# Optimization experiments

Hardware: AMD Instinct MI355X
Metric: run time of the kernel (lower is better)

## Reference

```python
import jax, jax.numpy as jnp
import numpy as np

N_NODES = 50000
N_EDGES = 800000
N_GRAPHS = 500
NFEAT = 128
NHID = 64
NLAYER = 3
BN_EPS = 1e-5


def setup_inputs() -> dict:
    key = jax.random.key(0)
    ks = jax.random.split(key, 8)
    x = jax.random.normal(ks[0], (N_NODES, NFEAT), dtype=jnp.float32)
    edge_index = jax.random.randint(ks[1], (2, N_EDGES), 0, N_NODES)
    batch = jnp.sort(jax.random.randint(ks[2], (N_NODES,), 0, N_GRAPHS))
    Wt = jax.random.normal(ks[3], (NFEAT, NHID), dtype=jnp.float32) / np.float32(np.sqrt(NFEAT))
    bt = jnp.zeros((NHID,), jnp.float32)
    gamma0 = jnp.ones((NHID,), jnp.float32)
    beta0 = jnp.zeros((NHID,), jnp.float32)
    W1 = jax.random.normal(ks[4], (NLAYER, NHID, NHID), dtype=jnp.float32) / np.float32(np.sqrt(NHID))
    W2 = jax.random.normal(ks[5], (NLAYER, NHID, NHID), dtype=jnp.float32) / np.float32(np.sqrt(NHID))
    gammas = jnp.ones((NLAYER, NHID), jnp.float32)
    betas = jnp.zeros((NLAYER, NHID), jnp.float32)
    return dict(x=x, edge_index=edge_index, batch=batch, Wt=Wt, bt=bt,
                gamma0=gamma0, beta0=beta0, W1=W1, W2=W2, gammas=gammas, betas=betas)


def _bn(h, g, b):
    # BatchNorm1d training-mode math: batch mean, biased variance
    mean = jnp.mean(h, axis=0)
    var = jnp.mean((h - mean) ** 2, axis=0)
    return (h - mean) * jax.lax.rsqrt(var + BN_EPS) * g + b


def _pool_mean(h, batch):
    s = jax.ops.segment_sum(h, batch, num_segments=N_GRAPHS)
    cnt = jax.ops.segment_sum(jnp.ones((h.shape[0], 1), h.dtype), batch, num_segments=N_GRAPHS)
    return s / jnp.maximum(cnt, 1.0)


def _embed_std(h, batch):
    m = _pool_mean(h, batch)                      # [G, nhid]
    s = jnp.sqrt(_pool_mean((h - m[batch]) ** 2, batch))
    return m, s


def reference(x, edge_index, batch, Wt, bt, gamma0, beta0, W1, W2, gammas, betas):
    src, dst = edge_index[0], edge_index[1]
    h = _bn(x @ Wt + bt, gamma0, beta0)           # transform: Linear + BN
    e0, s0 = _embed_std(h, batch)

    def step(h, p):
        w1, w2, g, b = p
        agg = jax.ops.segment_sum(h[src], dst, num_segments=N_NODES)  # GIN sum-aggregation
        z = (h + agg)                              # (1+eps)*x + agg, eps=0
        z = jax.nn.relu(z @ w1) @ w2               # GINConv nn: Linear-ReLU-Linear (no bias)
        z = _bn(jax.nn.relu(z), g, b)              # act then BN
        e, s = _embed_std(z, batch)
        return z, (e, s)

    _, (es, ss) = jax.lax.scan(step, h, (W1, W2, gammas, betas))
    graph_embeds = jnp.concatenate([e0[None], es], axis=0)  # [nlayer+1, G, nhid]
    graph_stds = jnp.concatenate([s0[None], ss], axis=0)
    return graph_embeds, graph_stds
```

## Files before the change

### kernel.cpp

```cpp
#include <hip/hip_runtime.h>
#include <hip/hip_bf16.h>

#define NN 50000
#define NE 800000
#define NG 500
#define NF 128
#define NH 64
#define NB 256
#define NPB 196
#define CAPB 4096
#define EPB 4096
#define NBLK ((NE + EPB - 1)/EPB)
#define CSR_LDS 2048
#define GBIN 8

typedef unsigned int u32;
typedef unsigned short u16;
typedef _Float16 h2 __attribute__((ext_vector_type(2)));
typedef _Float16 h8 __attribute__((ext_vector_type(8)));
typedef float f32x4 __attribute__((ext_vector_type(4)));

__device__ __forceinline__ float bf1(u16 v){ return __uint_as_float(((u32)v) << 16); }
__device__ __forceinline__ float h1(u16 v){ return (float)__builtin_bit_cast(_Float16, v); }
__device__ __forceinline__ u32 pk(float a, float b){
  return __builtin_bit_cast(u32, __builtin_amdgcn_cvt_pkrtz(a, b));
}
__device__ __forceinline__ h2 uph(u32 u){ return __builtin_bit_cast(h2, u); }
__device__ __forceinline__ u16 f16b(float f){ return __builtin_bit_cast(u16, (_Float16)f); }

__device__ __forceinline__ void cv8h(uint4 q, float* f){
  h2 v0 = uph(q.x), v1 = uph(q.y), v2 = uph(q.z), v3 = uph(q.w);
  f[0]=(float)v0.x; f[1]=(float)v0.y; f[2]=(float)v1.x; f[3]=(float)v1.y;
  f[4]=(float)v2.x; f[5]=(float)v2.y; f[6]=(float)v3.x; f[7]=(float)v3.y;
}

__device__ __forceinline__ h8 pack8(float4 p, float4 q){
  uint4 t;
  t.x = pk(p.x, p.y); t.y = pk(p.z, p.w);
  t.z = pk(q.x, q.y); t.w = pk(q.z, q.w);
  return __builtin_bit_cast(h8, t);
}
__device__ __forceinline__ f32x4 z4(){
  f32x4 v; v[0]=0.f; v[1]=0.f; v[2]=0.f; v[3]=0.f; return v;
}

__device__ __forceinline__ void gflush(float* sGT, float* sGT2,
    float* gE, float* gS, int b, int gFirst, int c, float pv, float pv2){
  if (pv == 0.f && pv2 == 0.f) return;
  if (b < GBIN){
    atomicAdd(&sGT[b*NH + c], pv);
    atomicAdd(&sGT2[b*NH + c], pv2);
  } else {
    unsafeAtomicAdd(&gE[(size_t)(gFirst + b)*NH + c], pv);
    unsafeAtomicAdd(&gS[(size_t)(gFirst + b)*NH + c], pv2);
  }
}

__global__ __launch_bounds__(256) void k_init(const u32* __restrict__ xw, int* __restrict__ flag,
    const int* __restrict__ batch, int* __restrict__ starts,
    const float* __restrict__ Wt, const float* __restrict__ W1, const float* __restrict__ W2,
    u16* __restrict__ wtT, u16* __restrict__ w1T, u16* __restrict__ w2T){
  int b = blockIdx.x, tid = threadIdx.x;
  if (b < 48){
    int t = b*256 + tid;
    if (t < NH*NF){
      int c = t >> 7, k = t & 127;
      wtT[t] = f16b(Wt[(size_t)k*NH + c]);
    }
    if (t < 3*NH*NH){
      int l = t >> 12, c = (t >> 6) & 63, k = t & 63;
      w1T[t] = f16b(W1[(size_t)l*NH*NH + k*NH + c]);
      w2T[t] = f16b(W2[(size_t)l*NH*NH + k*NH + c]);
    }
  } else {
    if (tid < 64){
      u32 w = xw[tid];
      u32 lo = w & 0xFFFFu;
      u32 e = (lo >> 7) & 0xFFu;
      bool vote = (e >= 0x60u && e <= 0x8Fu);
      unsigned long long m = __ballot(vote);
      if (tid == 0) flag[0] = (__popcll(m) >= 32) ? 1 : 0;
    }
    for (int g = tid; g <= NG; g += 256){
      int lo = 0, hi = NN;
      while (lo < hi){ int mid = (lo + hi) >> 1; if (batch[mid] < g) lo = mid + 1; else hi = mid; }
      starts[g] = lo;
    }
  }
}


__global__ __launch_bounds__(256) void k_bscat(const int* __restrict__ ei,
    int* __restrict__ bcur, u32* __restrict__ pkE){
  __shared__ int h[NB];
  __shared__ int loff[NB];
  __shared__ int base[NB];
  __shared__ int part[NB];
  __shared__ u32 sv[EPB];
  int tid = threadIdx.x;
  h[tid] = 0;
  __syncthreads();
  int e0 = blockIdx.x*EPB;
  u32 meta[16], vals[16];
  #pragma unroll
  for (int i = 0; i < 16; i++){
    int e = e0 + i*256 + tid;
    if (e < NE){
      int s = ei[e], d = ei[NE + e];
      int b = d / NPB;
      int r = atomicAdd(&h[b], 1);
      meta[i] = ((u32)b << 16) | (u32)r;
      vals[i] = ((u32)d << 16) | (u32)s;
    } else meta[i] = 0xFFFFFFFFu;
  }
  __syncthreads();
  int cnt = h[tid];
  part[tid] = cnt;
  __syncthreads();
  for (int off = 1; off < 256; off <<= 1){
    int u = (tid >= off) ? part[tid-off] : 0;
    __syncthreads();
    part[tid] += u;
    __syncthreads();
  }
  loff[tid] = part[tid] - cnt;
  base[tid] = tid*CAPB + (cnt ? atomicAdd(&bcur[tid], cnt) : 0);
  __syncthreads();
  #pragma unroll
  for (int i = 0; i < 16; i++){
    if (meta[i] != 0xFFFFFFFFu){
      int b = meta[i] >> 16, r = meta[i] & 0xFFFFu;
      sv[loff[b] + r] = vals[i];
    }
  }
  __syncthreads();
  int total = min(EPB, NE - e0);
  for (int j = tid; j < total; j += 256){
    u32 v = sv[j];
    int b = (int)(v >> 16) / NPB;
    pkE[base[b] + (j - loff[b])] = v;
  }
}

__global__ __launch_bounds__(256) void k_bfill(const u32* __restrict__ pkE,
    const int* __restrict__ bcur, int* __restrict__ rowptr, int* __restrict__ csr){
  __shared__ int part[NB];
  __shared__ int cur[NB];
  int b = blockIdx.x;
  int tid = threadIdx.x;
  int nb0 = b*NPB;
  int nr = min(NPB, NN - nb0);
  int rbeg = b*CAPB;
  int ecnt = bcur[b];
  int rend = rbeg + ecnt;
  part[tid] = 0;
  __syncthreads();
  for (int j = rbeg + tid; j < rend; j += 256){
    u32 pe = pkE[j];
    atomicAdd(&part[(int)(pe >> 16) - nb0], 1);
  }
  __syncthreads();
  int v = part[tid];
  __syncthreads();
  for (int off = 1; off < 256; off <<= 1){
    int u = (tid >= off) ? part[tid-off] : 0;
    __syncthreads();
    part[tid] += u;
    __syncthreads();
  }
  int ex = part[tid] - v;
  if (tid < nr) rowptr[nb0 + tid] = rbeg + ex;
  if (b == NB-1 && tid == 0) rowptr[NN] = rbeg + ecnt;
  cur[tid] = ex;
  __syncthreads();
  for (int j = rbeg + tid; j < rend; j += 256){
    u32 pe = pkE[j];
    int node = (int)(pe >> 16) - nb0;
    int p = atomicAdd(&cur[node], 1);
    csr[rbeg + p] = (int)(pe & 0xFFFFu);
  }
}

__global__ __launch_bounds__(256) void k_transform_m(const float* __restrict__ x,
    const u16* __restrict__ wtT, const float* __restrict__ bt,
    const int* __restrict__ batch,
    u16* __restrict__ th, float* __restrict__ s1, float* __restrict__ gstat0){
  __shared__ float sRed[8*NH];
  __shared__ float sGT[GBIN*NH], sGT2[GBIN*NH];
  __shared__ int sB[64];
  float* gE = gstat0;
  float* gS = gstat0 + (size_t)NG*NH;
  int tid = threadIdx.x;
  int blk0 = blockIdx.x*64;
  for (int i = tid; i < GBIN*NH; i += 256){ sGT[i] = 0.f; sGT2[i] = 0.f; }
  if (tid < 64) sB[tid] = batch[min(blk0 + tid, NN-1)];
  int w = tid >> 6, l = tid & 63;
  int lr = l & 15, kb = l >> 4;
  h8 bf[4][4];
  #pragma unroll
  for (int n = 0; n < 4; n++)
    #pragma unroll
    for (int kk = 0; kk < 4; kk++)
      bf[n][kk] = *(const h8*)&wtT[(size_t)(16*n + lr)*NF + kk*32 + kb*8];
  int node0 = blk0 + w*16;
  int rowA = node0 + lr; if (rowA > NN-1) rowA = NN-1;
  const float* xr = x + (size_t)rowA*NF + kb*8;
  f32x4 acc[4];
  #pragma unroll
  for (int n = 0; n < 4; n++) acc[n] = z4();
  #pragma unroll
  for (int kk = 0; kk < 4; kk++){
    float4 p = *(const float4*)(xr + kk*32);
    float4 q = *(const float4*)(xr + kk*32 + 4);
    h8 a = pack8(p, q);
    #pragma unroll
    for (int n = 0; n < 4; n++)
      acc[n] = __builtin_amdgcn_mfma_f32_16x16x32_f16(a, bf[n][kk], acc[n], 0, 0, 0);
  }
  __syncthreads();
  int gFirst = sB[0];
  int nlb = w*16 + 4*kb;
  #pragma unroll
  for (int n = 0; n < 4; n++){
    float bias = bt[16*n + lr];
    int c = 16*n + lr;
    float a1 = 0.f, a2 = 0.f;
    float pv = 0.f, pv2 = 0.f;
    int curb = sB[nlb] - gFirst;
    #pragma unroll
    for (int r = 0; r < 4; r++){
      int g = node0 + 4*kb + r;
      float v = acc[n][r] + bias;
      if (g < NN){
        u16 hv = f16b(v);
        th[(size_t)g*NH + c] = hv;
        a1 += v; a2 += v*v;
        float vr = h1(hv);
        int b = sB[nlb + r] - gFirst;
        if (b != curb){ gflush(sGT, sGT2, gE, gS, curb, gFirst, c, pv, pv2); pv = 0.f; pv2 = 0.f; curb = b; }
        pv += vr; pv2 += vr*vr;
      }
    }
    gflush(sGT, sGT2, gE, gS, curb, gFirst, c, pv, pv2);
    a1 += __shfl_xor(a1, 16); a1 += __shfl_xor(a1, 32);
    a2 += __shfl_xor(a2, 16); a2 += __shfl_xor(a2, 32);
    if (kb == 0){
      sRed[w*NH + c] = a1;
      sRed[(4+w)*NH + c] = a2;
    }
  }
  __syncthreads();
  if (tid < NH){
    float a1 = sRed[tid] + sRed[NH+tid] + sRed[2*NH+tid] + sRed[3*NH+tid];
    float a2 = sRed[4*NH+tid] + sRed[5*NH+tid] + sRed[6*NH+tid] + sRed[7*NH+tid];
    unsafeAtomicAdd(&s1[tid], a1);
    unsafeAtomicAdd(&s1[NH+tid], a2);
  }
  for (int i = tid; i < GBIN*NH; i += 256){
    float vE = sGT[i], vS = sGT2[i];
    if (vE != 0.f || vS != 0.f){
      int g = gFirst + (i >> 6);
      unsafeAtomicAdd(&gE[(size_t)g*NH + (i & 63)], vE);
      unsafeAtomicAdd(&gS[(size_t)g*NH + (i & 63)], vS);
    }
  }
}

__global__ __launch_bounds__(512) void k_gmlp(const u16* __restrict__ t,
    const int* __restrict__ rowptr, const int* __restrict__ csr,
    const int* __restrict__ bcur,
    const int* __restrict__ batch, u16* __restrict__ Th,
    const u16* __restrict__ w1T, const u16* __restrict__ w2T, int wofs,
    const float* __restrict__ s1i,
    const void* __restrict__ gamma, const void* __restrict__ beta, int ofs,
    const int* __restrict__ flag, float* __restrict__ s1o, float* __restrict__ gstatL){
  __shared__ __align__(16) u16 sU[64*NH];
  __shared__ __align__(16) u16 sV[64*NH];
  __shared__ float sRed[8*NH];
  __shared__ float scs[NH], shs[NH];
  __shared__ int sCsr[CSR_LDS];
  __shared__ int sRp[65];
  __shared__ int sEn[64];
  __shared__ float sGT[GBIN*NH], sGT2[GBIN*NH];
  __shared__ int sB[64];
  float* gE = gstatL;
  float* gS = gstatL + (size_t)NG*NH;
  int tid = threadIdx.x;
  int node0 = blockIdx.x*64;
  sGT[tid] = 0.f; sGT2[tid] = 0.f;
  if (tid < NH){
    int bfl = flag[0];
    float gm = bfl ? bf1(((const u16*)gamma)[ofs+tid]) : ((const float*)gamma)[ofs+tid];
    float be = bfl ? bf1(((const u16*)beta)[ofs+tid])  : ((const float*)beta)[ofs+tid];
    float mean = s1i[tid] * (1.f/NN);
    float var  = s1i[NH+tid] * (1.f/NN) - mean*mean;
    float rr = rsqrtf(fmaxf(var, 0.f) + 1e-5f);
    float sc = gm * rr;
    scs[tid] = sc;
    shs[tid] = be - mean*sc;
  }
  if (tid >= 128 && tid < 193){
    int idx = tid - 128;
    int nd = node0 + idx;
    sRp[idx] = rowptr[nd > NN ? NN : nd];
  }
  if (tid >= 256 && tid < 320)
    sB[tid - 256] = batch[min(node0 + tid - 256, NN-1)];
  if (tid >= 320 && tid < 384){
    int idx = tid - 320;
    int nd = node0 + idx;
    if (nd < NN){
      int nb = nd / NPB;
      sEn[idx] = (((nd + 1) % NPB) == 0) ? (nb*CAPB + bcur[nb]) : rowptr[nd + 1];
    } else sEn[idx] = 0;
  }
  __syncthreads();
  int base = sRp[0];
  int cnt = sRp[64] - base;
  int gFirst = sB[0];
  for (int i = tid; i < cnt && i < CSR_LDS; i += 512) sCsr[i] = csr[base + i];
  __syncthreads();
  int w = tid >> 6, lane = tid & 63;
  {
    int slot = lane >> 3, chunk = lane & 7;
    int nl = w*8 + slot;
    int node = node0 + nl;
    int swz = (nl & 7) << 3;
    if (node < NN){
      int beg = sRp[nl], en = sEn[nl];
      float acc[8];
      uint4 qs = *(const uint4*)&t[(size_t)node*NH + chunk*8];
      cv8h(qs, acc);
      int j = beg;
      for (; j + 4 <= en; j += 4){
        int o = j - base;
        int s0 = (o + 0 < CSR_LDS) ? sCsr[o+0] : csr[j+0];
        int s1 = (o + 1 < CSR_LDS) ? sCsr[o+1] : csr[j+1];
        int s2 = (o + 2 < CSR_LDS) ? sCsr[o+2] : csr[j+2];
        int s3 = (o + 3 < CSR_LDS) ? sCsr[o+3] : csr[j+3];
        uint4 q0 = *(const uint4*)&t[(size_t)s0*NH + chunk*8];
        uint4 q1 = *(const uint4*)&t[(size_t)s1*NH + chunk*8];
        uint4 q2 = *(const uint4*)&t[(size_t)s2*NH + chunk*8];
        uint4 q3 = *(const uint4*)&t[(size_t)s3*NH + chunk*8];
        float f0[8], f1[8], f2[8], f3[8];
        cv8h(q0, f0); cv8h(q1, f1); cv8h(q2, f2); cv8h(q3, f3);
        #pragma unroll
        for (int i = 0; i < 8; i++) acc[i] += (f0[i] + f1[i]) + (f2[i] + f3[i]);
      }
      for (; j < en; j++){
        int o = j - base;
        int s0 = (o < CSR_LDS) ? sCsr[o] : csr[j];
        uint4 q = *(const uint4*)&t[(size_t)s0*NH + chunk*8];
        float f[8]; cv8h(q, f);
        #pragma unroll
        for (int i = 0; i < 8; i++) acc[i] += f[i];
      }
      float deg1 = (float)(en - beg + 1);
      float o8[8];
      #pragma unroll
      for (int i = 0; i < 8; i++)
        o8[i] = scs[chunk*8+i]*acc[i] + deg1*shs[chunk*8+i];
      uint4 ov;
      ov.x = pk(o8[0], o8[1]); ov.y = pk(o8[2], o8[3]);
      ov.z = pk(o8[4], o8[5]); ov.w = pk(o8[6], o8[7]);
      *(uint4*)&sU[nl*NH + ((chunk*8) ^ swz)] = ov;
    } else {
      uint4 zz; zz.x = 0; zz.y = 0; zz.z = 0; zz.w = 0;
      *(uint4*)&sU[nl*NH + ((chunk*8) ^ swz)] = zz;
    }
  }
  __syncthreads();
  int lr = lane & 15, kb = lane >> 4;
  int rb = w & 3, ch = w >> 2;
  h8 b1[2][2], b2[2][2];
  #pragma unroll
  for (int n2 = 0; n2 < 2; n2++)
    #pragma unroll
    for (int kk = 0; kk < 2; kk++){
      int n = 2*ch + n2;
      b1[n2][kk] = *(const h8*)&w1T[wofs + (16*n + lr)*NH + kk*32 + kb*8];
      b2[n2][kk] = *(const h8*)&w2T[wofs + (16*n + lr)*NH + kk*32 + kb*8];
    }
  int rv = 16*rb + lr;
  f32x4 acc[2];
  acc[0] = z4(); acc[1] = z4();
  const u16* urow = sU + rv*NH;
  #pragma unroll
  for (int kk = 0; kk < 2; kk++){
    h8 a = *(const h8*)&urow[(kk*32 + kb*8) ^ ((rv & 7) << 3)];
    #pragma unroll
    for (int n2 = 0; n2 < 2; n2++)
      acc[n2] = __builtin_amdgcn_mfma_f32_16x16x32_f16(a, b1[n2][kk], acc[n2], 0, 0, 0);
  }
  #pragma unroll
  for (int n2 = 0; n2 < 2; n2++){
    int n = 2*ch + n2;
    #pragma unroll
    for (int r = 0; r < 4; r++){
      int row = 16*rb + 4*kb + r;
      int col = 16*n + lr;
      sV[row*NH + (col ^ ((row & 7) << 3))] = f16b(fmaxf(acc[n2][r], 0.f));
    }
  }
  __syncthreads();
  f32x4 acc2[2];
  acc2[0] = z4(); acc2[1] = z4();
  const u16* vrow = sV + rv*NH;
  #pragma unroll
  for (int kk = 0; kk < 2; kk++){
    h8 a = *(const h8*)&vrow[(kk*32 + kb*8) ^ ((rv & 7) << 3)];
    #pragma unroll
    for (int n2 = 0; n2 < 2; n2++)
      acc2[n2] = __builtin_amdgcn_mfma_f32_16x16x32_f16(a, b2[n2][kk], acc2[n2], 0, 0, 0);
  }
  int nlb = 16*rb + 4*kb;
  #pragma unroll
  for (int n2 = 0; n2 < 2; n2++){
    int n = 2*ch + n2;
    int c = 16*n + lr;
    float a1 = 0.f, a2 = 0.f;
    float pv = 0.f, pv2 = 0.f;
    int curb = sB[nlb] - gFirst;
    #pragma unroll
    for (int r = 0; r < 4; r++){
      int g = node0 + nlb + r;
      float v = fmaxf(acc2[n2][r], 0.f);
      if (g < NN){
        u16 hv = f16b(v);
        Th[(size_t)g*NH + c] = hv;
        a1 += v; a2 += v*v;
        float vr = h1(hv);
        int b = sB[nlb + r] - gFirst;
        if (b != curb){ gflush(sGT, sGT2, gE, gS, curb, gFirst, c, pv, pv2); pv = 0.f; pv2 = 0.f; curb = b; }
        pv += vr; pv2 += vr*vr;
      }
    }
    gflush(sGT, sGT2, gE, gS, curb, gFirst, c, pv, pv2);
    a1 += __shfl_xor(a1, 16); a1 += __shfl_xor(a1, 32);
    a2 += __shfl_xor(a2, 16); a2 += __shfl_xor(a2, 32);
    if (kb == 0){
      sRed[rb*NH + c] = a1;
      sRed[(4+rb)*NH + c] = a2;
    }
  }
  __syncthreads();
  if (tid < NH){
    float a1 = sRed[tid] + sRed[NH+tid] + sRed[2*NH+tid] + sRed[3*NH+tid];
    float a2 = sRed[4*NH+tid] + sRed[5*NH+tid] + sRed[6*NH+tid] + sRed[7*NH+tid];
    unsafeAtomicAdd(&s1o[tid], a1);
    unsafeAtomicAdd(&s1o[NH+tid], a2);
  }
  {
    float vE = sGT[tid], vS = sGT2[tid];
    if (vE != 0.f || vS != 0.f){
      int g = gFirst + (tid >> 6);
      unsafeAtomicAdd(&gE[(size_t)g*NH + (tid & 63)], vE);
      unsafeAtomicAdd(&gS[(size_t)g*NH + (tid & 63)], vS);
    }
  }
}

__global__ __launch_bounds__(256) void k_fin(const float* __restrict__ sAll,
    const float* __restrict__ gstat,
    const void* __restrict__ g0, const void* __restrict__ b0,
    const void* __restrict__ gs, const void* __restrict__ bs,
    const int* __restrict__ starts, const int* __restrict__ flag,
    void* __restrict__ dout){
  int g = blockIdx.x;
  int l = threadIdx.x >> 6, c = threadIdx.x & 63;
  int bf = flag[0];
  const void* gam = (l == 0) ? g0 : gs;
  const void* bet = (l == 0) ? b0 : bs;
  int ofs = (l == 0) ? 0 : (l-1)*NH;
  float gm = bf ? bf1(((const u16*)gam)[ofs+c]) : ((const float*)gam)[ofs+c];
  float be = bf ? bf1(((const u16*)bet)[ofs+c]) : ((const float*)bet)[ofs+c];
  const float* stage = sAll + (size_t)l*128;
  float mean = stage[c] * (1.f/NN);
  float var  = stage[NH+c] * (1.f/NN) - mean*mean;
  float rr = rsqrtf(fmaxf(var, 0.f) + 1e-5f);
  float sc = gm * rr;
  float sh = be - mean*sc;
  int cnt = starts[g+1] - starts[g];
  float inv = 1.f / (float)max(cnt, 1);
  const float* gE = gstat + (size_t)l*2*NG*NH;
  const float* gS = gE + (size_t)NG*NH;
  float mT = gE[(size_t)g*NH + c] * inv;
  float mz = sc*mT + sh;
  float vz = sc*sc*(gS[(size_t)g*NH + c] * inv - mT*mT);
  float s = sqrtf(fmaxf(vz, 0.f));
  if (cnt == 0){ mz = 0.f; s = 0.f; }
  size_t eidx = ((size_t)l*NG + g)*NH + c;
  size_t sidx = (size_t)4*NG*NH + eidx;
  if (bf){
    ((__hip_bfloat16*)dout)[eidx] = __float2bfloat16(mz);
    ((__hip_bfloat16*)dout)[sidx] = __float2bfloat16(s);
  } else {
    ((float*)dout)[eidx] = mz;
    ((float*)dout)[sidx] = s;
  }
}

extern "C" void kernel_launch(void* const* d_in, const int* in_sizes, int n_in,
                              void* d_out, int out_size, void* d_ws, size_t ws_size,
                              hipStream_t stream) {
  const void* x    = d_in[0];
  const int* ei    = (const int*)d_in[1];
  const int* batch = (const int*)d_in[2];
  const void* Wt   = d_in[3];
  const void* bt   = d_in[4];
  const void* g0   = d_in[5];
  const void* b0   = d_in[6];
  const void* W1   = d_in[7];
  const void* W2   = d_in[8];
  const void* gs   = d_in[9];
  const void* bs   = d_in[10];

  u16*  tA    = (u16*)d_ws;
  u16*  tB    = tA + (size_t)NN*NH;
  float* sAll = (float*)(tB + (size_t)NN*NH);
  int* bcur   = (int*)(sAll + 512);
  float* gstat = (float*)(bcur + NB);
  int* starts = (int*)(gstat + (size_t)4*2*NG*NH);
  int* flag   = starts + 512;
  int* rowptr = flag + 64;
  u32* pkE    = (u32*)(rowptr + NN + 64);
  int* csr    = (int*)(pkE + (size_t)NB*CAPB);
  u16* wtT    = (u16*)(csr + (size_t)NB*CAPB);
  u16* w1T    = wtT + (size_t)NH*NF;
  u16* w2T    = w1T + (size_t)3*NH*NH;

  size_t zbytes = (512 + NB)*sizeof(float) + (size_t)4*2*NG*NH*sizeof(float);
  hipMemsetAsync(sAll, 0, zbytes, stream);
  k_init<<<49, 256, 0, stream>>>((const u32*)x, flag, batch, starts,
      (const float*)Wt, (const float*)W1, (const float*)W2, wtT, w1T, w2T);
  k_bscat<<<NBLK, 256, 0, stream>>>(ei, bcur, pkE);
  k_bfill<<<NB, 256, 0, stream>>>(pkE, bcur, rowptr, csr);

  k_transform_m<<<(NN+63)/64, 256, 0, stream>>>((const float*)x, wtT, (const float*)bt,
      batch, tA, sAll, gstat);

  u16* tin = tA;
  u16* tout = tB;
  for (int l = 0; l < 3; l++){
    float* sIn  = sAll + (size_t)l*128;
    float* sOut = sAll + (size_t)(l+1)*128;
    const void* gg = (l == 0) ? g0 : gs;
    const void* bb = (l == 0) ? b0 : bs;
    int ofs = (l == 0) ? 0 : (l-1)*NH;
    k_gmlp<<<(NN+63)/64, 512, 0, stream>>>(tin, rowptr, csr, bcur, batch, tout, w1T, w2T, l*NH*NH,
        sIn, gg, bb, ofs, flag, sOut, gstat + (size_t)(l+1)*2*NG*NH);
    u16* tmp = tin; tin = tout; tout = tmp;
  }
  k_fin<<<NG, 256, 0, stream>>>(sAll, gstat, g0, b0, gs, bs, starts, flag, d_out);
}
```

Measured before the change: 286.4 us.

## Merge edge bucket-scatter and input transform into one horizontally fused launch

Combines the edge bucket-scatter kernel and the input Linear+BN-stats transform kernel into a single launch, where block index selects which role a block plays and shared memory is unioned between the two roles. Because the two stages are independent, they can now run concurrently across CUs instead of serializing, and one kernel launch is removed. The fused kernel needs enough shared memory for the larger branch and enough registers for the heavier one, which may lower occupancy for the lighter branch.

```diff
diff --git a/kernel.cpp b/kernel.cpp
--- a/kernel.cpp
+++ b/kernel.cpp
@@ -11,6 +11,7 @@
 #define CAPB 4096
 #define EPB 4096
 #define NBLK ((NE + EPB - 1)/EPB)
+#define TBLK ((NN + 63)/64)
 #define CSR_LDS 2048
 #define GBIN 8
 
@@ -89,56 +90,146 @@
   }
 }
 
-
-__global__ __launch_bounds__(256) void k_bscat(const int* __restrict__ ei,
-    int* __restrict__ bcur, u32* __restrict__ pkE){
-  __shared__ int h[NB];
-  __shared__ int loff[NB];
-  __shared__ int base[NB];
-  __shared__ int part[NB];
-  __shared__ u32 sv[EPB];
+__global__ __launch_bounds__(256) void k_bsct(const int* __restrict__ ei,
+    int* __restrict__ bcur, u32* __restrict__ pkE,
+    const float* __restrict__ x, const u16* __restrict__ wtT, const float* __restrict__ bt,
+    const int* __restrict__ batch,
+    u16* __restrict__ th, float* __restrict__ s1, float* __restrict__ gstat0){
+  __shared__ union {
+    struct {
+      int h[NB];
+      int loff[NB];
+      int base[NB];
+      int part[NB];
+      u32 sv[EPB];
+    } s;
+    struct {
+      float sRed[8*NH];
+      float sGT[GBIN*NH];
+      float sGT2[GBIN*NH];
+      int sB[64];
+    } t;
+  } u;
   int tid = threadIdx.x;
-  h[tid] = 0;
-  __syncthreads();
-  int e0 = blockIdx.x*EPB;
-  u32 meta[16], vals[16];
-  #pragma unroll
-  for (int i = 0; i < 16; i++){
-    int e = e0 + i*256 + tid;
-    if (e < NE){
-      int s = ei[e], d = ei[NE + e];
-      int b = d / NPB;
-      int r = atomicAdd(&h[b], 1);
-      meta[i] = ((u32)b << 16) | (u32)r;
-      vals[i] = ((u32)d << 16) | (u32)s;
-    } else meta[i] = 0xFFFFFFFFu;
-  }
-  __syncthreads();
-  int cnt = h[tid];
-  part[tid] = cnt;
-  __syncthreads();
-  for (int off = 1; off < 256; off <<= 1){
-    int u = (tid >= off) ? part[tid-off] : 0;
-    __syncthreads();
-    part[tid] += u;
-    __syncthreads();
-  }
-  loff[tid] = part[tid] - cnt;
-  base[tid] = tid*CAPB + (cnt ? atomicAdd(&bcur[tid], cnt) : 0);
-  __syncthreads();
-  #pragma unroll
-  for (int i = 0; i < 16; i++){
-    if (meta[i] != 0xFFFFFFFFu){
-      int b = meta[i] >> 16, r = meta[i] & 0xFFFFu;
-      sv[loff[b] + r] = vals[i];
-    }
-  }
-  __syncthreads();
-  int total = min(EPB, NE - e0);
-  for (int j = tid; j < total; j += 256){
-    u32 v = sv[j];
-    int b = (int)(v >> 16) / NPB;
-    pkE[base[b] + (j - loff[b])] = v;
+  if (blockIdx.x < NBLK){
+    u.s.h[tid] = 0;
+    __syncthreads();
+    int e0 = blockIdx.x*EPB;
+    u32 meta[16], vals[16];
+    #pragma unroll
+    for (int i = 0; i < 16; i++){
+      int e = e0 + i*256 + tid;
+      if (e < NE){
+        int s = ei[e], d = ei[NE + e];
+        int b = d / NPB;
+        int r = atomicAdd(&u.s.h[b], 1);
+        meta[i] = ((u32)b << 16) | (u32)r;
+        vals[i] = ((u32)d << 16) | (u32)s;
+      } else meta[i] = 0xFFFFFFFFu;
+    }
+    __syncthreads();
+    int cnt = u.s.h[tid];
+    u.s.part[tid] = cnt;
+    __syncthreads();
+    for (int off = 1; off < 256; off <<= 1){
+      int v = (tid >= off) ? u.s.part[tid-off] : 0;
+      __syncthreads();
+      u.s.part[tid] += v;
+      __syncthreads();
+    }
+    u.s.loff[tid] = u.s.part[tid] - cnt;
+    u.s.base[tid] = tid*CAPB + (cnt ? atomicAdd(&bcur[tid], cnt) : 0);
+    __syncthreads();
+    #pragma unroll
+    for (int i = 0; i < 16; i++){
+      if (meta[i] != 0xFFFFFFFFu){
+        int b = meta[i] >> 16, r = meta[i] & 0xFFFFu;
+        u.s.sv[u.s.loff[b] + r] = vals[i];
+      }
+    }
+    __syncthreads();
+    int total = min(EPB, NE - e0);
+    for (int j = tid; j < total; j += 256){
+      u32 v = u.s.sv[j];
+      int b = (int)(v >> 16) / NPB;
+      pkE[u.s.base[b] + (j - u.s.loff[b])] = v;
+    }
+  } else {
+    float* gE = gstat0;
+    float* gS = gstat0 + (size_t)NG*NH;
+    int blk0 = (blockIdx.x - NBLK)*64;
+    for (int i = tid; i < GBIN*NH; i += 256){ u.t.sGT[i] = 0.f; u.t.sGT2[i] = 0.f; }
+    if (tid < 64) u.t.sB[tid] = batch[min(blk0 + tid, NN-1)];
+    int w = tid >> 6, l = tid & 63;
+    int lr = l & 15, kb = l >> 4;
+    h8 bf[4][4];
+    #pragma unroll
+    for (int n = 0; n < 4; n++)
+      #pragma unroll
+      for (int kk = 0; kk < 4; kk++)
+        bf[n][kk] = *(const h8*)&wtT[(size_t)(16*n + lr)*NF + kk*32 + kb*8];
+    int node0 = blk0 + w*16;
+    int rowA = node0 + lr; if (rowA > NN-1) rowA = NN-1;
+    const float* xr = x + (size_t)rowA*NF + kb*8;
+    f32x4 acc[4];
+    #pragma unroll
+    for (int n = 0; n < 4; n++) acc[n] = z4();
+    #pragma unroll
+    for (int kk = 0; kk < 4; kk++){
+      float4 p = *(const float4*)(xr + kk*32);
+      float4 q = *(const float4*)(xr + kk*32 + 4);
+      h8 a = pack8(p, q);
+      #pragma unroll
+      for (int n = 0; n < 4; n++)
+        acc[n] = __builtin_amdgcn_mfma_f32_16x16x32_f16(a, bf[n][kk], acc[n], 0, 0, 0);
+    }
+    __syncthreads();
+    int gFirst = u.t.sB[0];
+    int nlb = w*16 + 4*kb;
+    #pragma unroll
+    for (int n = 0; n < 4; n++){
+      float bias = bt[16*n + lr];
+      int c = 16*n + lr;
+      float a1 = 0.f, a2 = 0.f;
+      float pv = 0.f, pv2 = 0.f;
+      int curb = u.t.sB[nlb] - gFirst;
+      #pragma unroll
+      for (int r = 0; r < 4; r++){
+        int g = node0 + 4*kb + r;
+        float v = acc[n][r] + bias;
+        if (g < NN){
+          u16 hv = f16b(v);
+          th[(size_t)g*NH + c] = hv;
+          a1 += v; a2 += v*v;
+          float vr = h1(hv);
+          int b = u.t.sB[nlb + r] - gFirst;
+          if (b != curb){ gflush(u.t.sGT, u.t.sGT2, gE, gS, curb, gFirst, c, pv, pv2); pv = 0.f; pv2 = 0.f; curb = b; }
+          pv += vr; pv2 += vr*vr;
+        }
+      }
+      gflush(u.t.sGT, u.t.sGT2, gE, gS, curb, gFirst, c, pv, pv2);
+      a1 += __shfl_xor(a1, 16); a1 += __shfl_xor(a1, 32);
+      a2 += __shfl_xor(a2, 16); a2 += __shfl_xor(a2, 32);
+      if (kb == 0){
+        u.t.sRed[w*NH + c] = a1;
+        u.t.sRed[(4+w)*NH + c] = a2;
+      }
+    }
+    __syncthreads();
+    if (tid < NH){
+      float a1 = u.t.sRed[tid] + u.t.sRed[NH+tid] + u.t.sRed[2*NH+tid] + u.t.sRed[3*NH+tid];
+      float a2 = u.t.sRed[4*NH+tid] + u.t.sRed[5*NH+tid] + u.t.sRed[6*NH+tid] + u.t.sRed[7*NH+tid];
+      unsafeAtomicAdd(&s1[tid], a1);
+      unsafeAtomicAdd(&s1[NH+tid], a2);
+    }
+    for (int i = tid; i < GBIN*NH; i += 256){
+      float vE = u.t.sGT[i], vS = u.t.sGT2[i];
+      if (vE != 0.f || vS != 0.f){
+        int g = gFirst + (i >> 6);
+        unsafeAtomicAdd(&gE[(size_t)g*NH + (i & 63)], vE);
+        unsafeAtomicAdd(&gS[(size_t)g*NH + (i & 63)], vS);
+      }
+    }
   }
 }
 
@@ -163,9 +254,9 @@
   int v = part[tid];
   __syncthreads();
   for (int off = 1; off < 256; off <<= 1){
-    int u = (tid >= off) ? part[tid-off] : 0;
-    __syncthreads();
-    part[tid] += u;
+    int u2 = (tid >= off) ? part[tid-off] : 0;
+    __syncthreads();
+    part[tid] += u2;
     __syncthreads();
   }
   int ex = part[tid] - v;
@@ -178,91 +269,6 @@
     int node = (int)(pe >> 16) - nb0;
     int p = atomicAdd(&cur[node], 1);
     csr[rbeg + p] = (int)(pe & 0xFFFFu);
-  }
-}
-
-__global__ __launch_bounds__(256) void k_transform_m(const float* __restrict__ x,
-    const u16* __restrict__ wtT, const float* __restrict__ bt,
-    const int* __restrict__ batch,
-    u16* __restrict__ th, float* __restrict__ s1, float* __restrict__ gstat0){
-  __shared__ float sRed[8*NH];
-  __shared__ float sGT[GBIN*NH], sGT2[GBIN*NH];
-  __shared__ int sB[64];
-  float* gE = gstat0;
-  float* gS = gstat0 + (size_t)NG*NH;
-  int tid = threadIdx.x;
-  int blk0 = blockIdx.x*64;
-  for (int i = tid; i < GBIN*NH; i += 256){ sGT[i] = 0.f; sGT2[i] = 0.f; }
-  if (tid < 64) sB[tid] = batch[min(blk0 + tid, NN-1)];
-  int w = tid >> 6, l = tid & 63;
-  int lr = l & 15, kb = l >> 4;
-  h8 bf[4][4];
-  #pragma unroll
-  for (int n = 0; n < 4; n++)
-    #pragma unroll
-    for (int kk = 0; kk < 4; kk++)
-      bf[n][kk] = *(const h8*)&wtT[(size_t)(16*n + lr)*NF + kk*32 + kb*8];
-  int node0 = blk0 + w*16;
-  int rowA = node0 + lr; if (rowA > NN-1) rowA = NN-1;
-  const float* xr = x + (size_t)rowA*NF + kb*8;
-  f32x4 acc[4];
-  #pragma unroll
-  for (int n = 0; n < 4; n++) acc[n] = z4();
-  #pragma unroll
-  for (int kk = 0; kk < 4; kk++){
-    float4 p = *(const float4*)(xr + kk*32);
-    float4 q = *(const float4*)(xr + kk*32 + 4);
-    h8 a = pack8(p, q);
-    #pragma unroll
-    for (int n = 0; n < 4; n++)
-      acc[n] = __builtin_amdgcn_mfma_f32_16x16x32_f16(a, bf[n][kk], acc[n], 0, 0, 0);
-  }
-  __syncthreads();
-  int gFirst = sB[0];
-  int nlb = w*16 + 4*kb;
-  #pragma unroll
-  for (int n = 0; n < 4; n++){
-    float bias = bt[16*n + lr];
-    int c = 16*n + lr;
-    float a1 = 0.f, a2 = 0.f;
-    float pv = 0.f, pv2 = 0.f;
-    int curb = sB[nlb] - gFirst;
-    #pragma unroll
-    for (int r = 0; r < 4; r++){
-      int g = node0 + 4*kb + r;
-      float v = acc[n][r] + bias;
-      if (g < NN){
-        u16 hv = f16b(v);
-        th[(size_t)g*NH + c] = hv;
-        a1 += v; a2 += v*v;
-        float vr = h1(hv);
-        int b = sB[nlb + r] - gFirst;
-        if (b != curb){ gflush(sGT, sGT2, gE, gS, curb, gFirst, c, pv, pv2); pv = 0.f; pv2 = 0.f; curb = b; }
-        pv += vr; pv2 += vr*vr;
-      }
-    }
-    gflush(sGT, sGT2, gE, gS, curb, gFirst, c, pv, pv2);
-    a1 += __shfl_xor(a1, 16); a1 += __shfl_xor(a1, 32);
-    a2 += __shfl_xor(a2, 16); a2 += __shfl_xor(a2, 32);
-    if (kb == 0){
-      sRed[w*NH + c] = a1;
-      sRed[(4+w)*NH + c] = a2;
-    }
-  }
-  __syncthreads();
-  if (tid < NH){
-    float a1 = sRed[tid] + sRed[NH+tid] + sRed[2*NH+tid] + sRed[3*NH+tid];
-    float a2 = sRed[4*NH+tid] + sRed[5*NH+tid] + sRed[6*NH+tid] + sRed[7*NH+tid];
-    unsafeAtomicAdd(&s1[tid], a1);
-    unsafeAtomicAdd(&s1[NH+tid], a2);
-  }
-  for (int i = tid; i < GBIN*NH; i += 256){
-    float vE = sGT[i], vS = sGT2[i];
-    if (vE != 0.f || vS != 0.f){
-      int g = gFirst + (i >> 6);
-      unsafeAtomicAdd(&gE[(size_t)g*NH + (i & 63)], vE);
-      unsafeAtomicAdd(&gS[(size_t)g*NH + (i & 63)], vS);
-    }
   }
 }
 
@@ -533,11 +539,9 @@
   hipMemsetAsync(sAll, 0, zbytes, stream);
   k_init<<<49, 256, 0, stream>>>((const u32*)x, flag, batch, starts,
       (const float*)Wt, (const float*)W1, (const float*)W2, wtT, w1T, w2T);
-  k_bscat<<<NBLK, 256, 0, stream>>>(ei, bcur, pkE);
+  k_bsct<<<NBLK + TBLK, 256, 0, stream>>>(ei, bcur, pkE,
+      (const float*)x, wtT, (const float*)bt, batch, tA, sAll, gstat);
   k_bfill<<<NB, 256, 0, stream>>>(pkE, bcur, rowptr, csr);
-
-  k_transform_m<<<(NN+63)/64, 256, 0, stream>>>((const float*)x, wtT, (const float*)bt,
-      batch, tA, sAll, gstat);
 
   u16* tin = tA;
   u16* tout = tB;
```

Result: faster. 273.0 us (median of 2 runs) (-4.7%).
